# Kernel optimization log

Hardware: AMD Instinct MI355X
Metric: run time of the kernel (lower is better)

Reference implementation:

```python
import jax, jax.numpy as jnp
import numpy as np

K = 5          # top-k for surrogate precision
T1 = 1.0       # temperature for the top-k gate sigmoid
T2 = 0.01      # temperature for the soft-rank sigmoid
BIG = 1e6      # large finite distance for ignored (self) pairs


def setup_inputs() -> dict:
    key = jax.random.key(0)
    k1, k2 = jax.random.split(key)
    emb = jax.random.normal(k1, (512, 384), dtype=jnp.float32)
    labels = jax.random.randint(k2, (512,), 0, 64)
    return {"emb": emb, "labels": labels}


def _surrogate_precision_loss(emb, labels):
    bs = emb.shape[0]
    # pairwise euclidean distances (every sample is both query and gallery)
    sq = jnp.sum(emb * emb, axis=1)
    d2 = sq[:, None] + sq[None, :] - 2.0 * (emb @ emb.T)
    dist = jnp.sqrt(jnp.maximum(d2, 1e-12))                 # (Q, G)
    # ignore query-vs-itself pairs (diagonal)
    ignore = jnp.eye(bs, dtype=bool)
    mask_gt = (labels[:, None] == labels[None, :]) & ~ignore  # (Q, G)
    dist = jnp.where(ignore, BIG, dist)                     # push self to last rank
    # soft rank: rank[q, j] = sum_m sigmoid((d[q, j] - d[q, m]) / t2)
    diff = dist[:, :, None] - dist[:, None, :]              # (Q, G, G)
    rank = jax.nn.sigmoid(diff / T2).sum(axis=-1)           # (Q, G)
    gt = mask_gt.astype(dist.dtype)
    # soft precision@k per query, normalized by min(#gt, k)
    num = (jax.nn.sigmoid((K - rank) / T1) * gt).sum(axis=1)
    den = jnp.minimum(gt.sum(axis=1), jnp.asarray(K, dist.dtype))
    precision = num / den
    return 1.0 - precision.mean()


def reference(emb, labels):
    return _surrogate_precision_loss(emb, labels)
```

## Files before the change

### kernel.cpp

```cpp
#include <hip/hip_runtime.h>
#include <hip/hip_bf16.h>

#define N 512
#define D 384
#define TILE 32
#define BK 128
#define LDSTRIDE (BK + 4)

#if __has_builtin(__builtin_amdgcn_exp2f)
#define EXP2F(x) __builtin_amdgcn_exp2f(x)
#else
#define EXP2F(x) exp2f(x)
#endif
#if __has_builtin(__builtin_amdgcn_rcpf)
#define RCPF(x) __builtin_amdgcn_rcpf(x)
#else
#define RCPF(x) (1.0f / (x))
#endif

__global__ __launch_bounds__(256) void dist_kernel(const float* __restrict__ emb,
                                                   float* __restrict__ dist) {
    __shared__ float As[TILE][LDSTRIDE];
    __shared__ float Bs[TILE][LDSTRIDE];
    const int bi = blockIdx.y;
    const int bj = blockIdx.x;
    const int t  = threadIdx.x;
    const int tc = t & 15;
    const int tr = t >> 4;
    const int rowBase = bi * TILE;
    const int colBase = bj * TILE;

    float d00 = 0.f, d01 = 0.f, d10 = 0.f, d11 = 0.f;

    for (int kk = 0; kk < D; kk += BK) {
#pragma unroll
        for (int i = 0; i < 4; ++i) {
            int f  = t + i * 256;
            int r  = f >> 5;
            int c4 = f & 31;
            float4 va = *((const float4*)(emb + (rowBase + r) * D + kk) + c4);
            *((float4*)&As[r][c4 * 4]) = va;
            float4 vb = *((const float4*)(emb + (colBase + r) * D + kk) + c4);
            *((float4*)&Bs[r][c4 * 4]) = vb;
        }
        __syncthreads();
#pragma unroll
        for (int k4 = 0; k4 < BK / 4; ++k4) {
            float4 a0 = *((const float4*)&As[tr][k4 * 4]);
            float4 a1 = *((const float4*)&As[tr + 16][k4 * 4]);
            float4 b0 = *((const float4*)&Bs[tc][k4 * 4]);
            float4 b1 = *((const float4*)&Bs[tc + 16][k4 * 4]);
            float e;
            e = a0.x - b0.x; d00 += e * e;  e = a0.y - b0.y; d00 += e * e;
            e = a0.z - b0.z; d00 += e * e;  e = a0.w - b0.w; d00 += e * e;
            e = a0.x - b1.x; d01 += e * e;  e = a0.y - b1.y; d01 += e * e;
            e = a0.z - b1.z; d01 += e * e;  e = a0.w - b1.w; d01 += e * e;
            e = a1.x - b0.x; d10 += e * e;  e = a1.y - b0.y; d10 += e * e;
            e = a1.z - b0.z; d10 += e * e;  e = a1.w - b0.w; d10 += e * e;
            e = a1.x - b1.x; d11 += e * e;  e = a1.y - b1.y; d11 += e * e;
            e = a1.z - b1.z; d11 += e * e;  e = a1.w - b1.w; d11 += e * e;
        }
        __syncthreads();
    }

    const int r0 = rowBase + tr, r1 = rowBase + tr + 16;
    const int c0 = colBase + tc, c1 = colBase + tc + 16;
    float v00 = sqrtf(fmaxf(d00, 1e-12f));
    float v01 = sqrtf(fmaxf(d01, 1e-12f));
    float v10 = sqrtf(fmaxf(d10, 1e-12f));
    float v11 = sqrtf(fmaxf(d11, 1e-12f));
    if (r0 == c0) v00 = 1e6f;
    if (r0 == c1) v01 = 1e6f;
    if (r1 == c0) v10 = 1e6f;
    if (r1 == c1) v11 = 1e6f;
    dist[r0 * N + c0] = v00;
    dist[r0 * N + c1] = v01;
    dist[r1 * N + c0] = v10;
    dist[r1 * N + c1] = v11;
}

__global__ __launch_bounds__(256) void loss_kernel(const float* __restrict__ dist,
                                                   const int* __restrict__ labels,
                                                   float* __restrict__ prec) {
    const int q = blockIdx.x;
    const int t = threadIdx.x;
    const int lane = t & 63, wave = t >> 6;
    __shared__ float s[N];
    __shared__ int gt_idx[N];
    __shared__ int gt_n;
    __shared__ float wnum[4];

    if (t == 0) gt_n = 0;
    __syncthreads();

    const int lq = labels[q];
    const float C = 144.26950408889634f;
    {
        const int j0 = t, j1 = t + 256;
        s[j0] = dist[q * N + j0] * C;
        s[j1] = dist[q * N + j1] * C;
        if (labels[j0] == lq && j0 != q) { int p = atomicAdd(&gt_n, 1); gt_idx[p] = j0; }
        if (labels[j1] == lq && j1 != q) { int p = atomicAdd(&gt_n, 1); gt_idx[p] = j1; }
    }
    __syncthreads();

    const int n = gt_n;
    float mynum = 0.f;
    for (int i = wave; i < n; i += 4) {
        const float sj = s[gt_idx[i]];
        float r = 0.f;
#pragma unroll
        for (int m = lane; m < N; m += 64) {
            r += RCPF(1.f + EXP2F(s[m] - sj));
        }
#pragma unroll
        for (int off = 32; off > 0; off >>= 1) r += __shfl_down(r, off);
        if (lane == 0) {
            mynum += RCPF(1.f + EXP2F((r - 5.f) * 1.4426950408889634f));
        }
    }
    if (lane == 0) wnum[wave] = mynum;
    __syncthreads();
    if (t == 0) {
        float tot = wnum[0] + wnum[1] + wnum[2] + wnum[3];
        float den = fminf((float)n, 5.f);
        prec[q] = tot / den;
    }
}

__global__ __launch_bounds__(256) void final_kernel(const float* __restrict__ prec,
                                                    float* __restrict__ out) {
    const int t = threadIdx.x;
    const int lane = t & 63, wave = t >> 6;
    __shared__ float w[4];
    float v = prec[t] + prec[t + 256];
#pragma unroll
    for (int off = 32; off > 0; off >>= 1) v += __shfl_down(v, off);
    if (lane == 0) w[wave] = v;
    __syncthreads();
    if (t == 0) out[0] = 1.0f - (w[0] + w[1] + w[2] + w[3]) * (1.0f / 512.0f);
}

extern "C" void kernel_launch(void* const* d_in, const int* in_sizes, int n_in,
                              void* d_out, int out_size, void* d_ws, size_t ws_size,
                              hipStream_t stream) {
    const float* emb  = (const float*)d_in[0];
    const int* labels = (const int*)d_in[1];
    float* out        = (float*)d_out;
    char* ws          = (char*)d_ws;

    float* dist = (float*)ws;
    float* prec = (float*)(ws + (size_t)N * N * 4);

    hipLaunchKernelGGL(dist_kernel, dim3(N / TILE, N / TILE), dim3(256), 0, stream,
                       emb, dist);
    hipLaunchKernelGGL(loss_kernel, dim3(N), dim3(256), 0, stream, dist, labels, prec);
    hipLaunchKernelGGL(final_kernel, dim3(1), dim3(256), 0, stream, prec, out);
}
```

Before: 75.15 us.

## Fuse distance computation into loss kernel, two queries per block

Result: slower. 88.61 us (+17.9%).

```diff
diff --git a/kernel.cpp b/kernel.cpp
--- a/kernel.cpp
+++ b/kernel.cpp
@@ -1,11 +1,8 @@
 #include <hip/hip_runtime.h>
-#include <hip/hip_bf16.h>
 
 #define N 512
 #define D 384
-#define TILE 32
-#define BK 128
-#define LDSTRIDE (BK + 4)
+#define NF4 (D / 4)
 
 #if __has_builtin(__builtin_amdgcn_exp2f)
 #define EXP2F(x) __builtin_amdgcn_exp2f(x)
@@ -18,113 +15,79 @@
 #define RCPF(x) (1.0f / (x))
 #endif
 
-__global__ __launch_bounds__(256) void dist_kernel(const float* __restrict__ emb,
-                                                   float* __restrict__ dist) {
-    __shared__ float As[TILE][LDSTRIDE];
-    __shared__ float Bs[TILE][LDSTRIDE];
-    const int bi = blockIdx.y;
-    const int bj = blockIdx.x;
-    const int t  = threadIdx.x;
-    const int tc = t & 15;
-    const int tr = t >> 4;
-    const int rowBase = bi * TILE;
-    const int colBase = bj * TILE;
-
-    float d00 = 0.f, d01 = 0.f, d10 = 0.f, d11 = 0.f;
-
-    for (int kk = 0; kk < D; kk += BK) {
-#pragma unroll
-        for (int i = 0; i < 4; ++i) {
-            int f  = t + i * 256;
-            int r  = f >> 5;
-            int c4 = f & 31;
-            float4 va = *((const float4*)(emb + (rowBase + r) * D + kk) + c4);
-            *((float4*)&As[r][c4 * 4]) = va;
-            float4 vb = *((const float4*)(emb + (colBase + r) * D + kk) + c4);
-            *((float4*)&Bs[r][c4 * 4]) = vb;
-        }
-        __syncthreads();
-#pragma unroll
-        for (int k4 = 0; k4 < BK / 4; ++k4) {
-            float4 a0 = *((const float4*)&As[tr][k4 * 4]);
-            float4 a1 = *((const float4*)&As[tr + 16][k4 * 4]);
-            float4 b0 = *((const float4*)&Bs[tc][k4 * 4]);
-            float4 b1 = *((const float4*)&Bs[tc + 16][k4 * 4]);
-            float e;
-            e = a0.x - b0.x; d00 += e * e;  e = a0.y - b0.y; d00 += e * e;
-            e = a0.z - b0.z; d00 += e * e;  e = a0.w - b0.w; d00 += e * e;
-            e = a0.x - b1.x; d01 += e * e;  e = a0.y - b1.y; d01 += e * e;
-            e = a0.z - b1.z; d01 += e * e;  e = a0.w - b1.w; d01 += e * e;
-            e = a1.x - b0.x; d10 += e * e;  e = a1.y - b0.y; d10 += e * e;
-            e = a1.z - b0.z; d10 += e * e;  e = a1.w - b0.w; d10 += e * e;
-            e = a1.x - b1.x; d11 += e * e;  e = a1.y - b1.y; d11 += e * e;
-            e = a1.z - b1.z; d11 += e * e;  e = a1.w - b1.w; d11 += e * e;
-        }
-        __syncthreads();
-    }
-
-    const int r0 = rowBase + tr, r1 = rowBase + tr + 16;
-    const int c0 = colBase + tc, c1 = colBase + tc + 16;
-    float v00 = sqrtf(fmaxf(d00, 1e-12f));
-    float v01 = sqrtf(fmaxf(d01, 1e-12f));
-    float v10 = sqrtf(fmaxf(d10, 1e-12f));
-    float v11 = sqrtf(fmaxf(d11, 1e-12f));
-    if (r0 == c0) v00 = 1e6f;
-    if (r0 == c1) v01 = 1e6f;
-    if (r1 == c0) v10 = 1e6f;
-    if (r1 == c1) v11 = 1e6f;
-    dist[r0 * N + c0] = v00;
-    dist[r0 * N + c1] = v01;
-    dist[r1 * N + c0] = v10;
-    dist[r1 * N + c1] = v11;
-}
-
-__global__ __launch_bounds__(256) void loss_kernel(const float* __restrict__ dist,
-                                                   const int* __restrict__ labels,
-                                                   float* __restrict__ prec) {
-    const int q = blockIdx.x;
+__global__ __launch_bounds__(512) void fused_kernel(const float* __restrict__ emb,
+                                                    const int* __restrict__ labels,
+                                                    float* __restrict__ prec) {
+    const int b = blockIdx.x;
     const int t = threadIdx.x;
     const int lane = t & 63, wave = t >> 6;
-    __shared__ float s[N];
-    __shared__ int gt_idx[N];
-    __shared__ int gt_n;
-    __shared__ float wnum[4];
+    const int q0 = b, q1 = b + 256;
 
-    if (t == 0) gt_n = 0;
+    __shared__ float s0[N];
+    __shared__ float s1[N];
+    __shared__ float4 eq0[NF4];
+    __shared__ float4 eq1[NF4];
+    __shared__ short gt0[N], gt1[N];
+    __shared__ int n0, n1;
+    __shared__ float wnum[8];
+
+    if (t == 0) { n0 = 0; n1 = 0; }
+    const float4* embf4 = (const float4*)emb;
+    if (t < NF4)            eq0[t]        = embf4[(size_t)q0 * NF4 + t];
+    else if (t < 2 * NF4)   eq1[t - NF4]  = embf4[(size_t)q1 * NF4 + (t - NF4)];
     __syncthreads();
 
-    const int lq = labels[q];
+    float a0 = 0.f, a1 = 0.f;
+    const float4* rowp = embf4 + (size_t)t * NF4;
+#pragma unroll 8
+    for (int k = 0; k < NF4; ++k) {
+        float4 v  = rowp[k];
+        float4 u0 = eq0[k];
+        float4 u1 = eq1[k];
+        float e;
+        e = v.x - u0.x; a0 += e * e;  e = v.y - u0.y; a0 += e * e;
+        e = v.z - u0.z; a0 += e * e;  e = v.w - u0.w; a0 += e * e;
+        e = v.x - u1.x; a1 += e * e;  e = v.y - u1.y; a1 += e * e;
+        e = v.z - u1.z; a1 += e * e;  e = v.w - u1.w; a1 += e * e;
+    }
     const float C = 144.26950408889634f;
-    {
-        const int j0 = t, j1 = t + 256;
-        s[j0] = dist[q * N + j0] * C;
-        s[j1] = dist[q * N + j1] * C;
-        if (labels[j0] == lq && j0 != q) { int p = atomicAdd(&gt_n, 1); gt_idx[p] = j0; }
-        if (labels[j1] == lq && j1 != q) { int p = atomicAdd(&gt_n, 1); gt_idx[p] = j1; }
-    }
+    float d0 = sqrtf(fmaxf(a0, 1e-12f)) * C;
+    float d1 = sqrtf(fmaxf(a1, 1e-12f)) * C;
+    if (t == q0) d0 = 1e6f * C;
+    if (t == q1) d1 = 1e6f * C;
+    s0[t] = d0;
+    s1[t] = d1;
+
+    const int lt  = labels[t];
+    const int lq0 = labels[q0], lq1 = labels[q1];
+    if (lt == lq0 && t != q0) { int p = atomicAdd(&n0, 1); gt0[p] = (short)t; }
+    if (lt == lq1 && t != q1) { int p = atomicAdd(&n1, 1); gt1[p] = (short)t; }
     __syncthreads();
 
-    const int n = gt_n;
+    const float* s  = (wave < 4) ? s0 : s1;
+    const short* gt = (wave < 4) ? gt0 : gt1;
+    const int    n  = (wave < 4) ? n0 : n1;
+    const int    wq = wave & 3;
     float mynum = 0.f;
-    for (int i = wave; i < n; i += 4) {
-        const float sj = s[gt_idx[i]];
+    for (int i = wq; i < n; i += 4) {
+        const float sj = s[gt[i]];
         float r = 0.f;
 #pragma unroll
-        for (int m = lane; m < N; m += 64) {
+        for (int m = lane; m < N; m += 64)
             r += RCPF(1.f + EXP2F(s[m] - sj));
-        }
 #pragma unroll
         for (int off = 32; off > 0; off >>= 1) r += __shfl_down(r, off);
-        if (lane == 0) {
+        if (lane == 0)
             mynum += RCPF(1.f + EXP2F((r - 5.f) * 1.4426950408889634f));
-        }
     }
     if (lane == 0) wnum[wave] = mynum;
     __syncthreads();
     if (t == 0) {
-        float tot = wnum[0] + wnum[1] + wnum[2] + wnum[3];
-        float den = fminf((float)n, 5.f);
-        prec[q] = tot / den;
+        float num0 = wnum[0] + wnum[1] + wnum[2] + wnum[3];
+        prec[q0] = num0 / fminf((float)n0, 5.f);
+    } else if (t == 64) {
+        float num1 = wnum[4] + wnum[5] + wnum[6] + wnum[7];
+        prec[q1] = num1 / fminf((float)n1, 5.f);
     }
 }
 
@@ -147,13 +110,9 @@
     const float* emb  = (const float*)d_in[0];
     const int* labels = (const int*)d_in[1];
     float* out        = (float*)d_out;
-    char* ws          = (char*)d_ws;
+    float* prec       = (float*)d_ws;
 
-    float* dist = (float*)ws;
-    float* prec = (float*)(ws + (size_t)N * N * 4);
-
-    hipLaunchKernelGGL(dist_kernel, dim3(N / TILE, N / TILE), dim3(256), 0, stream,
-                       emb, dist);
-    hipLaunchKernelGGL(loss_kernel, dim3(N), dim3(256), 0, stream, dist, labels, prec);
+    hipLaunchKernelGGL(fused_kernel, dim3(N / 2), dim3(512), 0, stream,
+                       emb, labels, prec);
     hipLaunchKernelGGL(final_kernel, dim3(1), dim3(256), 0, stream, prec, out);
 }
```
